# Performance work log

Hardware: AMD Instinct MI355X
Metric: run time of the kernel (lower is better)

Reference implementation:

```python
import jax, jax.numpy as jnp
import numpy as np

B, T, C, NH = 1, 2048, 1024, 16
HS = C // NH            # 64
LEVEL = 6
LMIN = 2 ** LEVEL       # 64 (tail block size)
NB = T // LMIN          # 32 complete sets


def setup_inputs() -> dict:
    key = jax.random.key(0)
    ks = jax.random.split(key, 8)
    def w(k, shape, fan_in):
        return jax.random.normal(k, shape, jnp.float32) / np.sqrt(fan_in)
    return {
        "x": jax.random.normal(ks[0], (B, T, C), jnp.float32),
        "Wq": w(ks[1], (C, C), C),
        "Wk": w(ks[2], (C, C), C),
        "Wv": w(ks[3], (C, C), C),
        "Wkmap": w(ks[4], (HS, HS * HS), HS * HS),
        "bkmap": jnp.zeros((HS,), jnp.float32),
        "Wvmap": w(ks[5], (HS, HS * HS), HS * HS),
        "bvmap": jnp.zeros((HS,), jnp.float32),
        "Wc": w(ks[6], (C, C), C),
        "bc": jnp.zeros((C,), jnp.float32),
    }


def reference(x, Wq, Wk, Wv, Wkmap, bkmap, Wvmap, bvmap, Wc, bc):
    phi = lambda t: jax.nn.elu(t) + 1.0  # feature_map='elu'
    # preprocess: projections + feature map (no q/k normalization)
    q = phi((x @ Wq.T).reshape(B, T, NH, HS))
    k = phi((x @ Wk.T).reshape(B, T, NH, HS))
    v = (x @ Wv.T).reshape(B, T, NH, HS)

    # per-position outer products k_t (x) v_t, grouped into LMIN-sized blocks
    op = jnp.einsum('bthd,bthe->bthde', k, v).reshape(B, NB, LMIN, NH, HS, HS)
    # set feature = final state of linear-attn recurrence over each full block
    set_f = op.sum(axis=2).reshape(B, NB, NH, HS * HS)            # [B,NB,NH,HS^2]
    # tail feature at t = state over [t - t%LMIN, t] = in-block prefix cumsum
    tail_f = jnp.cumsum(op, axis=2).reshape(B, T, NH, HS * HS)    # [B,T,NH,HS^2]

    K = set_f @ Wkmap.T + bkmap      # [B,NB,NH,HS] (k_mapping=True)
    V = set_f @ Wvmap.T + bvmap      # [B,NB,NH,HS] (v_mapping=True)
    K_tail = tail_f @ Wkmap.T + bkmap  # [B,T,NH,HS]
    V_tail = tail_f @ Wvmap.T + bvmap  # [B,T,NH,HS]

    scale = 1.0 / np.sqrt(HS)
    logits = jnp.einsum('bthd,bshd->bhts', q, K) * scale          # [B,NH,T,NB]
    # query t may attend only complete sets strictly before its own block
    mask = jnp.arange(NB)[None, :] < (jnp.arange(T) // LMIN)[:, None]  # [T,NB]
    logits = jnp.where(mask[None, None], logits, -jnp.inf)
    tail_logit = (jnp.einsum('bthd,bthd->bth', q, K_tail) * scale)
    tail_logit = tail_logit.transpose(0, 2, 1)[..., None]         # [B,NH,T,1]

    att = jax.nn.softmax(jnp.concatenate([logits, tail_logit], axis=-1), axis=-1)
    out = (jnp.einsum('bhts,bshd->bhtd', att[..., :-1], V)
           + att[..., -1:] * V_tail.transpose(0, 2, 1, 3))        # [B,NH,T,HS]
    out = out.transpose(0, 2, 1, 3).reshape(B, T, C)
    return out @ Wc.T + bc
```

## Files before the change

### kernel.cpp

```cpp
#include <hip/hip_runtime.h>
#include <hip/hip_bf16.h>
#include <math.h>

typedef __hip_bfloat16 bf16;
typedef __attribute__((ext_vector_type(8))) short short8;
typedef __attribute__((ext_vector_type(4))) float f32x4;

#define C_DIM 1024
#define NHEAD 16
#define HS 64

__device__ __forceinline__ float bf2f(bf16 x) { return __bfloat162float(x); }
__device__ __forceinline__ short bfbits(float x) {
    bf16 h = __float2bfloat16(x);
    return *reinterpret_cast<short*>(&h);
}

__device__ __forceinline__ void gl16(const void* g, void* l) {
    __builtin_amdgcn_global_load_lds(
        (const __attribute__((address_space(1))) unsigned int*)g,
        (__attribute__((address_space(3))) unsigned int*)l, 16, 0, 0);
}

__device__ __forceinline__ void split8(const float* p, short8& h, short8& l) {
    float4 f0 = reinterpret_cast<const float4*>(p)[0];
    float4 f1 = reinterpret_cast<const float4*>(p)[1];
    float vals[8] = {f0.x, f0.y, f0.z, f0.w, f1.x, f1.y, f1.z, f1.w};
#pragma unroll
    for (int j = 0; j < 8; ++j) {
        bf16 hb = __float2bfloat16(vals[j]);
        float r = vals[j] - __bfloat162float(hb);
        h[j] = *reinterpret_cast<short*>(&hb);
        bf16 lb = __float2bfloat16(r);
        l[j] = *reinterpret_cast<short*>(&lb);
    }
}

__device__ __forceinline__ short8* tchunk(bf16* tile, int row, int ch) {
    return reinterpret_cast<short8*>(tile + row * 64 + (((ch) ^ (row & 7)) << 3));
}

__global__ __launch_bounds__(256) void presplit_all_kernel(
    const float* __restrict__ x, const float* __restrict__ Wq,
    const float* __restrict__ Wk, const float* __restrict__ Wv,
    bf16* __restrict__ xh, bf16* __restrict__ xl,
    bf16* __restrict__ wqh, bf16* __restrict__ wql,
    bf16* __restrict__ wkh, bf16* __restrict__ wkl,
    bf16* __restrict__ wvh, bf16* __restrict__ wvl)
{
    int blk = blockIdx.x;
    const float* src; bf16 *dh, *dl; long off;
    if (blk < 1024)      { src = x;  dh = xh;  dl = xl;  off = (long)blk * 2048; }
    else if (blk < 1536) { src = Wq; dh = wqh; dl = wql; off = (long)(blk - 1024) * 2048; }
    else if (blk < 2048) { src = Wk; dh = wkh; dl = wkl; off = (long)(blk - 1536) * 2048; }
    else                 { src = Wv; dh = wvh; dl = wvl; off = (long)(blk - 2048) * 2048; }
    long p = off + threadIdx.x * 8;
    int j = (int)(((p >> 3) ^ (p >> 10)) & 7);
    long dp = (p & ~56l) | ((long)j << 3);
    short8 h8, l8;
    split8(&src[p], h8, l8);
    *reinterpret_cast<short8*>(&dh[dp]) = h8;
    *reinterpret_cast<short8*>(&dl[dp]) = l8;
}

__global__ __launch_bounds__(256) void presplit_wc_kernel(
    const float* __restrict__ Wc, bf16* __restrict__ wch, bf16* __restrict__ wcl)
{
    long p = (long)blockIdx.x * 2048 + threadIdx.x * 8;
    int j = (int)(((p >> 3) ^ (p >> 10)) & 7);
    long dp = (p & ~56l) | ((long)j << 3);
    short8 h8, l8;
    split8(&Wc[p], h8, l8);
    *reinterpret_cast<short8*>(&wch[dp]) = h8;
    *reinterpret_cast<short8*>(&wcl[dp]) = l8;
}

__global__ __launch_bounds__(256) void presplit_wmap_kernel(
    const float* __restrict__ WK, const float* __restrict__ WV, bf16* __restrict__ Wm4)
{
    int d = blockIdx.x;
    int row = threadIdx.x >> 2, e0 = (threadIdx.x & 3) * 16;
    int sw0 = (((e0 >> 3) + 0) ^ (row & 7)) & 7;
    int sw1 = (((e0 >> 3) + 1) ^ (row & 7)) & 7;
    const float* pk = &WK[(long)row * 4096 + d * 64 + e0];
    const float* pv = &WV[(long)row * 4096 + d * 64 + e0];
    long bKh = ((long)(d * 4 + 0) * 64 + row) * 64;
    long bKl = ((long)(d * 4 + 1) * 64 + row) * 64;
    long bVh = ((long)(d * 4 + 2) * 64 + row) * 64;
    long bVl = ((long)(d * 4 + 3) * 64 + row) * 64;
    short8 h8, l8;
    split8(pk, h8, l8);     *(short8*)&Wm4[bKh + sw0*8] = h8; *(short8*)&Wm4[bKl + sw0*8] = l8;
    split8(pk + 8, h8, l8); *(short8*)&Wm4[bKh + sw1*8] = h8; *(short8*)&Wm4[bKl + sw1*8] = l8;
    split8(pv, h8, l8);     *(short8*)&Wm4[bVh + sw0*8] = h8; *(short8*)&Wm4[bVl + sw0*8] = l8;
    split8(pv + 8, h8, l8); *(short8*)&Wm4[bVh + sw1*8] = h8; *(short8*)&Wm4[bVl + sw1*8] = l8;
}

__global__ __launch_bounds__(256) void qkv_kernel(
    const bf16* __restrict__ xh, const bf16* __restrict__ xl,
    const bf16* __restrict__ wqh, const bf16* __restrict__ wql,
    const bf16* __restrict__ wkh, const bf16* __restrict__ wkl,
    const bf16* __restrict__ wvh, const bf16* __restrict__ wvl,
    float* __restrict__ qkv, float* __restrict__ kTg)
{
    __shared__ bf16 lds[32768];
    const int tid = threadIdx.x;
    const int lane = tid & 63, wid = tid >> 6;
    const int wr = wid >> 1, wc = wid & 1;
    const int proj = blockIdx.x >> 3;
    const int n0 = (blockIdx.x & 7) * 128;
    const int m0 = blockIdx.y * 128;
    const bf16* Bhp = proj == 0 ? wqh : (proj == 1 ? wkh : wvh);
    const bf16* Blp = proj == 0 ? wql : (proj == 1 ? wkl : wvl);
    float* C = qkv + (long)proj * 2097152;
    char* lb = reinterpret_cast<char*>(lds);

    f32x4 acc[4][4] = {};
    for (int kt = 0; kt < 16; ++kt) {
        const int k0 = kt << 6;
#pragma unroll
        for (int i = 0; i < 4; ++i) {
            int cc = tid + i * 256;
            int row = cc >> 3, j = cc & 7;
            long soA = (long)(m0 + row) * 1024 + k0 + j * 8;
            long soB = (long)(n0 + row) * 1024 + k0 + j * 8;
            gl16(&xh[soA],  lb + cc * 16);
            gl16(&xl[soA],  lb + 16384 + cc * 16);
            gl16(&Bhp[soB], lb + 32768 + cc * 16);
            gl16(&Blp[soB], lb + 49152 + cc * 16);
        }
        __syncthreads();
#pragma unroll
        for (int kk = 0; kk < 2; ++kk) {
            short8 afh[4], afl[4], bfh[4], bfl[4];
#pragma unroll
            for (int t = 0; t < 4; ++t) {
                int ra = wr * 64 + t * 16 + (lane & 15);
                int rb = wc * 64 + t * 16 + (lane & 15);
                int ch = kk * 4 + (lane >> 4);
                afh[t] = *tchunk(lds, ra, ch);
                afl[t] = *tchunk(lds + 8192, ra, ch);
                bfh[t] = *tchunk(lds + 16384, rb, ch);
                bfl[t] = *tchunk(lds + 24576, rb, ch);
            }
#pragma unroll
            for (int tm = 0; tm < 4; ++tm)
#pragma unroll
                for (int tn = 0; tn < 4; ++tn) {
                    acc[tm][tn] = __builtin_amdgcn_mfma_f32_16x16x32_bf16(
                        afh[tm], bfh[tn], acc[tm][tn], 0, 0, 0);
                    acc[tm][tn] = __builtin_amdgcn_mfma_f32_16x16x32_bf16(
                        afh[tm], bfl[tn], acc[tm][tn], 0, 0, 0);
                    acc[tm][tn] = __builtin_amdgcn_mfma_f32_16x16x32_bf16(
                        afl[tm], bfh[tn], acc[tm][tn], 0, 0, 0);
                }
        }
        __syncthreads();
    }
    if (proj == 1) {
        float* lf = reinterpret_cast<float*>(lds) + wid * 4096;
#pragma unroll
        for (int tm = 0; tm < 4; ++tm)
#pragma unroll
            for (int tn = 0; tn < 4; ++tn)
#pragma unroll
                for (int r = 0; r < 4; ++r) {
                    int s = tm * 16 + (lane >> 4) * 4 + r;
                    int dd = tn * 16 + (lane & 15);
                    float v = acc[tm][tn][r];
                    v = v > 0.f ? v + 1.f : __expf(v);
                    lf[dd * 64 + (s ^ dd)] = v;
                }
        asm volatile("s_waitcnt lgkmcnt(0)" ::: "memory");
        __builtin_amdgcn_sched_barrier(0);
        int pair = (blockIdx.y * 2 + wr) * 16 + ((blockIdx.x & 7) * 2 + wc);
        long pb = (long)pair * 4096;
        int s0 = (lane & 15) * 4;
#pragma unroll
        for (int ii = 0; ii < 16; ++ii) {
            int dd = (lane >> 4) * 16 + ii;
            float4 o;
            o.x = lf[dd * 64 + ((s0 + 0) ^ dd)];
            o.y = lf[dd * 64 + ((s0 + 1) ^ dd)];
            o.z = lf[dd * 64 + ((s0 + 2) ^ dd)];
            o.w = lf[dd * 64 + ((s0 + 3) ^ dd)];
            *reinterpret_cast<float4*>(&kTg[pb + (long)dd * 64 + s0]) = o;
        }
    } else {
#pragma unroll
        for (int tm = 0; tm < 4; ++tm)
#pragma unroll
            for (int tn = 0; tn < 4; ++tn)
#pragma unroll
                for (int r = 0; r < 4; ++r) {
                    int row = m0 + wr * 64 + tm * 16 + (lane >> 4) * 4 + r;
                    int col = n0 + wc * 64 + tn * 16 + (lane & 15);
                    float v = acc[tm][tn][r];
                    if (proj == 0) v = v > 0.f ? v + 1.f : __expf(v);
                    C[(long)row * 1024 + col] = v;
                }
    }
}

__global__ __launch_bounds__(512, 4) void setfeat_kernel(
    const float* __restrict__ kTg, const float* __restrict__ vbuf,
    const bf16* __restrict__ Wm4,
    const float* __restrict__ bkmap, const float* __restrict__ bvmap,
    float* __restrict__ Ktail, float* __restrict__ Vtail,
    float* __restrict__ KsetT, float* __restrict__ Vset)
{
    __shared__ char smem[65536];
    bf16* W0 = reinterpret_cast<bf16*>(smem);
    bf16* W1 = reinterpret_cast<bf16*>(smem + 32768);
    const int tid = threadIdx.x;
    const int grp = tid >> 8, tl = tid & 255;
    const int lane = tl & 63, wid = tl >> 6;
    const int wr = wid >> 1, wc = wid & 1;
    const int pairIdx = blockIdx.x * 2 + grp;
    const int b = pairIdx >> 4, h = pairIdx & 15;
    const long base_kv = ((long)b * 64) * C_DIM + h * HS;
    const float* kp = kTg + (long)pairIdx * 4096;

    float vv0[2][8], vv1[2][8];
#pragma unroll
    for (int kk = 0; kk < 2; ++kk) {
        const float* p0 = &vbuf[base_kv +
            (long)(wr * 32 + (lane & 15)) * C_DIM + kk * 32 + (lane >> 4) * 8];
        const float* p1 = &vbuf[base_kv +
            (long)(wr * 32 + 16 + (lane & 15)) * C_DIM + kk * 32 + (lane >> 4) * 8];
        *reinterpret_cast<float4*>(&vv0[kk][0]) = reinterpret_cast<const float4*>(p0)[0];
        *reinterpret_cast<float4*>(&vv0[kk][4]) = reinterpret_cast<const float4*>(p0)[1];
        *reinterpret_cast<float4*>(&vv1[kk][0]) = reinterpret_cast<const float4*>(p1)[0];
        *reinterpret_cast<float4*>(&vv1[kk][4]) = reinterpret_cast<const float4*>(p1)[1];
    }
    float ks0 = kp[wr * 32 + (lane & 15)];
    float ks1 = kp[wr * 32 + 16 + (lane & 15)];
#pragma unroll
    for (int i = 0; i < 4; ++i) {
        int cc = tid + i * 512;
        gl16(&Wm4[(long)cc * 8], smem + (long)cc * 16);
    }
    f32x4 accK[2][2] = {}, accV[2][2] = {};

    for (int d = 0; d < 64; ++d) {
        bf16* Wcur = (d & 1) ? W1 : W0;
        char* Wnxt = (d & 1) ? smem : smem + 32768;
        __builtin_amdgcn_s_barrier();
        float kn0 = 0.f, kn1 = 0.f;
        if (d < 63) {
            kn0 = kp[(d + 1) * 64 + wr * 32 + (lane & 15)];
            kn1 = kp[(d + 1) * 64 + wr * 32 + 16 + (lane & 15)];
#pragma unroll
            for (int i = 0; i < 4; ++i) {
                int cc = tid + i * 512;
                gl16(&Wm4[(long)(d + 1) * 16384 + (long)cc * 8], Wnxt + (long)cc * 16);
            }
            asm volatile("s_waitcnt vmcnt(6)" ::: "memory");
        } else {
            asm volatile("s_waitcnt vmcnt(0)" ::: "memory");
        }
#pragma unroll
        for (int kk = 0; kk < 2; ++kk) {
            short8 bkh[2], bkl[2], bvh[2], bvl[2];
#pragma unroll
            for (int t = 0; t < 2; ++t) {
                int rb = wc * 32 + t * 16 + (lane & 15);
                int ch = kk * 4 + (lane >> 4);
                bkh[t] = *tchunk(Wcur,         rb, ch);
                bkl[t] = *tchunk(Wcur + 4096,  rb, ch);
                bvh[t] = *tchunk(Wcur + 8192,  rb, ch);
                bvl[t] = *tchunk(Wcur + 12288, rb, ch);
            }
            short8 a0, a1;
#pragma unroll
            for (int j = 0; j < 8; ++j) {
                a0[j] = bfbits(ks0 * vv0[kk][j]);
                a1[j] = bfbits(ks1 * vv1[kk][j]);
            }
#pragma unroll
            for (int tn = 0; tn < 2; ++tn) {
                accK[0][tn] = __builtin_amdgcn_mfma_f32_16x16x32_bf16(a0, bkh[tn], accK[0][tn], 0, 0, 0);
                accK[0][tn] = __builtin_amdgcn_mfma_f32_16x16x32_bf16(a0, bkl[tn], accK[0][tn], 0, 0, 0);
                accK[1][tn] = __builtin_amdgcn_mfma_f32_16x16x32_bf16(a1, bkh[tn], accK[1][tn], 0, 0, 0);
                accK[1][tn] = __builtin_amdgcn_mfma_f32_16x16x32_bf16(a1, bkl[tn], accK[1][tn], 0, 0, 0);
                accV[0][tn] = __builtin_amdgcn_mfma_f32_16x16x32_bf16(a0, bvh[tn], accV[0][tn], 0, 0, 0);
                accV[0][tn] = __builtin_amdgcn_mfma_f32_16x16x32_bf16(a0, bvl[tn], accV[0][tn], 0, 0, 0);
                accV[1][tn] = __builtin_amdgcn_mfma_f32_16x16x32_bf16(a1, bvh[tn], accV[1][tn], 0, 0, 0);
                accV[1][tn] = __builtin_amdgcn_mfma_f32_16x16x32_bf16(a1, bvl[tn], accV[1][tn], 0, 0, 0);
            }
        }
        ks0 = kn0; ks1 = kn1;
    }
    __syncthreads();
    float(*WallK)[64] = reinterpret_cast<float(*)[64]>(smem + grp * 32768);
    float(*WallV)[64] = reinterpret_cast<float(*)[64]>(smem + grp * 32768 + 16384);
#pragma unroll
    for (int tm = 0; tm < 2; ++tm)
#pragma unroll
        for (int tn = 0; tn < 2; ++tn)
#pragma unroll
            for (int r = 0; r < 4; ++r) {
                int row = wr * 32 + tm * 16 + (lane >> 4) * 4 + r;
                int col = wc * 32 + tn * 16 + (lane & 15);
                WallK[row][col] = (tm == 0 ? accK[0][tn][r] : accK[1][tn][r]);
                WallV[row][col] = (tm == 0 ? accV[0][tn][r] : accV[1][tn][r]);
            }
    __syncthreads();
    if (tl < 128) {
        int i = tl & 63;
        bool isV = tl >= 64;
        const float bi = isV ? bvmap[i] : bkmap[i];
        float run = 0.f;
        for (int s = 0; s < 64; ++s) {
            run += isV ? WallV[s][i] : WallK[s][i];
            float val = run + bi;
            long t = (long)b * 64 + s;
            if (isV) Vtail[t * C_DIM + h * HS + i] = val;
            else     Ktail[t * C_DIM + h * HS + i] = val;
            if (s == 63) {
                if (isV) Vset[(b * NHEAD + h) * HS + i] = val;
                else     KsetT[h * 2048 + i * 32 + b] = val;
            }
        }
    }
}

__global__ __launch_bounds__(256) void attn_kernel(
    const float* __restrict__ qbuf, const float* __restrict__ KsetT,
    const float* __restrict__ Vset, const float* __restrict__ Ktail,
    const float* __restrict__ Vtail, bf16* __restrict__ atth, bf16* __restrict__ attl)
{
    __shared__ float qsh[4][64];
    __shared__ float attsh[4][64];
    const int tid = threadIdx.x, lane = tid & 63, wid = tid >> 6;
    const int g = blockIdx.x * 4 + wid;
    const int t = g >> 4, h = g & 15;
    const int nb = t >> 6;
    const float scale = 0.125f;
    const long qoff = (long)t * C_DIM + h * HS;
    float qv = qbuf[qoff + lane];
    qsh[wid][lane] = qv;
    float tp = qv * Ktail[qoff + lane];
    for (int off = 32; off; off >>= 1) tp += __shfl_xor(tp, off, 64);
    __syncthreads();
    float logit = -INFINITY;
    if (lane < nb) {
        float s = 0.f;
        const float* Kp = &KsetT[h * 2048 + lane];
        for (int d = 0; d < 64; ++d) s += qsh[wid][d] * Kp[d * 32];
        logit = s * scale;
    } else if (lane == nb) {
        logit = tp * scale;
    }
    float m = logit;
    for (int off = 32; off; off >>= 1) m = fmaxf(m, __shfl_xor(m, off, 64));
    float e = (lane <= nb) ? __expf(logit - m) : 0.f;
    float sum = e;
    for (int off = 32; off; off >>= 1) sum += __shfl_xor(sum, off, 64);
    attsh[wid][lane] = e / sum;
    __syncthreads();
    float out = 0.f;
    for (int s = 0; s < nb; ++s)
        out += attsh[wid][s] * Vset[(s * NHEAD + h) * HS + lane];
    out += attsh[wid][nb] * Vtail[qoff + lane];
    bf16 hb = __float2bfloat16(out);
    int csw = (((lane >> 3) ^ (t & 7)) << 3) | (lane & 7);
    long po = (long)t * 1024 + h * 64 + csw;
    atth[po] = hb;
    attl[po] = __float2bfloat16(out - bf2f(hb));
}

__global__ __launch_bounds__(256) void gemm_final_kernel(
    const bf16* __restrict__ ah, const bf16* __restrict__ al,
    const bf16* __restrict__ bh, const bf16* __restrict__ bl,
    const float* __restrict__ bias, float* __restrict__ C)
{
    __shared__ bf16 lds[24576];
    const int tid = threadIdx.x;
    const int lane = tid & 63, wid = tid >> 6;
    const int wr = wid >> 1, wc = wid & 1;
    const int m0 = blockIdx.y * 128, n0 = blockIdx.x * 64;
    char* lb = reinterpret_cast<char*>(lds);

    f32x4 acc[4][2] = {};
    for (int kt = 0; kt < 16; ++kt) {
        const int k0 = kt << 6;
#pragma unroll
        for (int i = 0; i < 4; ++i) {
            int cc = tid + i * 256;
            int row = cc >> 3, j = cc & 7;
            long so = (long)(m0 + row) * 1024 + k0 + j * 8;
            gl16(&ah[so], lb + cc * 16);
            gl16(&al[so], lb + 16384 + cc * 16);
        }
#pragma unroll
        for (int i = 0; i < 2; ++i) {
            int cc = tid + i * 256;
            int row = cc >> 3, j = cc & 7;
            long so = (long)(n0 + row) * 1024 + k0 + j * 8;
            gl16(&bh[so], lb + 32768 + cc * 16);
            gl16(&bl[so], lb + 40960 + cc * 16);
        }
        __syncthreads();
#pragma unroll
        for (int kk = 0; kk < 2; ++kk) {
            short8 afh[4], afl[4], bfh[2], bfl[2];
#pragma unroll
            for (int t = 0; t < 4; ++t) {
                int ra = wr * 64 + t * 16 + (lane & 15);
                int ch = kk * 4 + (lane >> 4);
                afh[t] = *tchunk(lds, ra, ch);
                afl[t] = *tchunk(lds + 8192, ra, ch);
            }
#pragma unroll
            for (int t = 0; t < 2; ++t) {
                int rb = wc * 32 + t * 16 + (lane & 15);
                int ch = kk * 4 + (lane >> 4);
                bfh[t] = *tchunk(lds + 16384, rb, ch);
                bfl[t] = *tchunk(lds + 20480, rb, ch);
            }
#pragma unroll
            for (int tm = 0; tm < 4; ++tm)
#pragma unroll
                for (int tn = 0; tn < 2; ++tn) {
                    acc[tm][tn] = __builtin_amdgcn_mfma_f32_16x16x32_bf16(
                        afh[tm], bfh[tn], acc[tm][tn], 0, 0, 0);
                    acc[tm][tn] = __builtin_amdgcn_mfma_f32_16x16x32_bf16(
                        afh[tm], bfl[tn], acc[tm][tn], 0, 0, 0);
                    acc[tm][tn] = __builtin_amdgcn_mfma_f32_16x16x32_bf16(
                        afl[tm], bfh[tn], acc[tm][tn], 0, 0, 0);
                }
        }
        __syncthreads();
    }
#pragma unroll
    for (int tm = 0; tm < 4; ++tm)
#pragma unroll
        for (int tn = 0; tn < 2; ++tn)
#pragma unroll
            for (int r = 0; r < 4; ++r) {
                int row = m0 + wr * 64 + tm * 16 + (lane >> 4) * 4 + r;
                int col = n0 + wc * 32 + tn * 16 + (lane & 15);
                C[(long)row * 1024 + col] = acc[tm][tn][r] + bias[col];
            }
}

extern "C" void kernel_launch(void* const* d_in, const int* in_sizes, int n_in,
                              void* d_out, int out_size, void* d_ws, size_t ws_size,
                              hipStream_t stream)
{
    const float* x     = (const float*)d_in[0];
    const float* Wq    = (const float*)d_in[1];
    const float* Wk    = (const float*)d_in[2];
    const float* Wv    = (const float*)d_in[3];
    const float* Wkmap = (const float*)d_in[4];
    const float* bkmap = (const float*)d_in[5];
    const float* Wvmap = (const float*)d_in[6];
    const float* bvmap = (const float*)d_in[7];
    const float* Wc    = (const float*)d_in[8];
    const float* bc    = (const float*)d_in[9];
    float* out = (float*)d_out;

    char* ws = (char*)d_ws;
    const long MB = 1l << 20;
    float* q   = (float*)(ws + 0 * MB);
    float* kTg = (float*)(ws + 8 * MB);
    float* v   = (float*)(ws + 16 * MB);
    bf16* xh   = (bf16*)(ws + 24 * MB);
    bf16* xl   = (bf16*)(ws + 28 * MB);
    bf16* wqh  = (bf16*)(ws + 32 * MB);
    bf16* wql  = (bf16*)(ws + 34 * MB);
    bf16* wkh  = (bf16*)(ws + 36 * MB);
    bf16* wkl  = (bf16*)(ws + 38 * MB);
    bf16* wvh  = (bf16*)(ws + 40 * MB);
    bf16* wvl  = (bf16*)(ws + 42 * MB);
    bf16* Wm4  = (bf16*)(ws + 44 * MB);
    float* Ktail = (float*)(ws + 24 * MB);
    float* Vtail = (float*)(ws + 32 * MB);
    float* KsetT = (float*)(ws + 40 * MB);
    float* Vset  = (float*)(ws + 41 * MB);
    bf16* atth   = (bf16*)(ws + 8 * MB);
    bf16* attl   = (bf16*)(ws + 12 * MB);
    bf16* wch    = (bf16*)(ws + 44 * MB);
    bf16* wcl    = (bf16*)(ws + 46 * MB);

    presplit_all_kernel<<<2560, 256, 0, stream>>>(x, Wq, Wk, Wv, xh, xl,
                                                  wqh, wql, wkh, wkl, wvh, wvl);
    presplit_wmap_kernel<<<64, 256, 0, stream>>>(Wkmap, Wvmap, Wm4);
    qkv_kernel<<<dim3(24, 16), 256, 0, stream>>>(xh, xl, wqh, wql, wkh, wkl,
                                                 wvh, wvl, q, kTg);
    setfeat_kernel<<<256, 512, 0, stream>>>(kTg, v, Wm4, bkmap, bvmap,
                                            Ktail, Vtail, KsetT, Vset);
    presplit_wc_kernel<<<512, 256, 0, stream>>>(Wc, wch, wcl);
    attn_kernel<<<8192, 256, 0, stream>>>(q, KsetT, Vset, Ktail, Vtail, atth, attl);
    gemm_final_kernel<<<dim3(16, 16), 256, 0, stream>>>(atth, attl, wch, wcl, bc, out);
}
```

Before: 258.7 us.

## Factor k out of set-feature GEMM and split K/V mapping across blocks

```diff
diff --git a/kernel.cpp b/kernel.cpp
--- a/kernel.cpp
+++ b/kernel.cpp
@@ -208,91 +208,98 @@
     float* __restrict__ Ktail, float* __restrict__ Vtail,
     float* __restrict__ KsetT, float* __restrict__ Vset)
 {
-    __shared__ char smem[65536];
+    __shared__ char smem[32768];
     bf16* W0 = reinterpret_cast<bf16*>(smem);
-    bf16* W1 = reinterpret_cast<bf16*>(smem + 32768);
+    bf16* W1 = reinterpret_cast<bf16*>(smem + 16384);
     const int tid = threadIdx.x;
+    const int side = blockIdx.x & 1;
     const int grp = tid >> 8, tl = tid & 255;
     const int lane = tl & 63, wid = tl >> 6;
     const int wr = wid >> 1, wc = wid & 1;
-    const int pairIdx = blockIdx.x * 2 + grp;
+    const int pairIdx = (blockIdx.x >> 1) * 2 + grp;
     const int b = pairIdx >> 4, h = pairIdx & 15;
     const long base_kv = ((long)b * 64) * C_DIM + h * HS;
     const float* kp = kTg + (long)pairIdx * 4096;
-
-    float vv0[2][8], vv1[2][8];
-#pragma unroll
-    for (int kk = 0; kk < 2; ++kk) {
-        const float* p0 = &vbuf[base_kv +
-            (long)(wr * 32 + (lane & 15)) * C_DIM + kk * 32 + (lane >> 4) * 8];
-        const float* p1 = &vbuf[base_kv +
-            (long)(wr * 32 + 16 + (lane & 15)) * C_DIM + kk * 32 + (lane >> 4) * 8];
-        *reinterpret_cast<float4*>(&vv0[kk][0]) = reinterpret_cast<const float4*>(p0)[0];
-        *reinterpret_cast<float4*>(&vv0[kk][4]) = reinterpret_cast<const float4*>(p0)[1];
-        *reinterpret_cast<float4*>(&vv1[kk][0]) = reinterpret_cast<const float4*>(p1)[0];
-        *reinterpret_cast<float4*>(&vv1[kk][4]) = reinterpret_cast<const float4*>(p1)[1];
-    }
-    float ks0 = kp[wr * 32 + (lane & 15)];
-    float ks1 = kp[wr * 32 + 16 + (lane & 15)];
-#pragma unroll
-    for (int i = 0; i < 4; ++i) {
+    const long wsideoff = (long)side * 8192;
+
+    short8 vh[2][2];
+#pragma unroll
+    for (int tm = 0; tm < 2; ++tm)
+#pragma unroll
+        for (int kk = 0; kk < 2; ++kk) {
+            const float* vp = &vbuf[base_kv +
+                (long)(wr * 32 + tm * 16 + (lane & 15)) * C_DIM + kk * 32 + (lane >> 4) * 8];
+            float4 f0 = reinterpret_cast<const float4*>(vp)[0];
+            float4 f1 = reinterpret_cast<const float4*>(vp)[1];
+            float vals[8] = {f0.x, f0.y, f0.z, f0.w, f1.x, f1.y, f1.z, f1.w};
+#pragma unroll
+            for (int j = 0; j < 8; ++j) vh[tm][kk][j] = bfbits(vals[j]);
+        }
+    f32x4 kvc[2];
+#pragma unroll
+    for (int tm = 0; tm < 2; ++tm)
+        kvc[tm] = *reinterpret_cast<const f32x4*>(
+            &kp[wr * 32 + tm * 16 + (lane >> 4) * 4]);
+#pragma unroll
+    for (int i = 0; i < 2; ++i) {
         int cc = tid + i * 512;
-        gl16(&Wm4[(long)cc * 8], smem + (long)cc * 16);
-    }
-    f32x4 accK[2][2] = {}, accV[2][2] = {};
+        gl16(&Wm4[wsideoff + (long)cc * 8], smem + (long)cc * 16);
+    }
+    f32x4 acc[2][2] = {};
+    __syncthreads();
 
     for (int d = 0; d < 64; ++d) {
         bf16* Wcur = (d & 1) ? W1 : W0;
-        char* Wnxt = (d & 1) ? smem : smem + 32768;
+        char* Wnxt = (d & 1) ? smem : smem + 16384;
         __builtin_amdgcn_s_barrier();
-        float kn0 = 0.f, kn1 = 0.f;
+        f32x4 kvn[2] = {};
         if (d < 63) {
-            kn0 = kp[(d + 1) * 64 + wr * 32 + (lane & 15)];
-            kn1 = kp[(d + 1) * 64 + wr * 32 + 16 + (lane & 15)];
-#pragma unroll
-            for (int i = 0; i < 4; ++i) {
+#pragma unroll
+            for (int i = 0; i < 2; ++i) {
                 int cc = tid + i * 512;
-                gl16(&Wm4[(long)(d + 1) * 16384 + (long)cc * 8], Wnxt + (long)cc * 16);
-            }
-            asm volatile("s_waitcnt vmcnt(6)" ::: "memory");
+                gl16(&Wm4[(long)(d + 1) * 16384 + wsideoff + (long)cc * 8],
+                     Wnxt + (long)cc * 16);
+            }
+#pragma unroll
+            for (int tm = 0; tm < 2; ++tm)
+                kvn[tm] = *reinterpret_cast<const f32x4*>(
+                    &kp[(d + 1) * 64 + wr * 32 + tm * 16 + (lane >> 4) * 4]);
+            asm volatile("s_waitcnt vmcnt(4)" ::: "memory");
         } else {
             asm volatile("s_waitcnt vmcnt(0)" ::: "memory");
         }
+        f32x4 G[2][2] = {};
 #pragma unroll
         for (int kk = 0; kk < 2; ++kk) {
-            short8 bkh[2], bkl[2], bvh[2], bvl[2];
+            short8 bh_[2], bl_[2];
 #pragma unroll
             for (int t = 0; t < 2; ++t) {
                 int rb = wc * 32 + t * 16 + (lane & 15);
                 int ch = kk * 4 + (lane >> 4);
-                bkh[t] = *tchunk(Wcur,         rb, ch);
-                bkl[t] = *tchunk(Wcur + 4096,  rb, ch);
-                bvh[t] = *tchunk(Wcur + 8192,  rb, ch);
-                bvl[t] = *tchunk(Wcur + 12288, rb, ch);
-            }
-            short8 a0, a1;
-#pragma unroll
-            for (int j = 0; j < 8; ++j) {
-                a0[j] = bfbits(ks0 * vv0[kk][j]);
-                a1[j] = bfbits(ks1 * vv1[kk][j]);
-            }
-#pragma unroll
-            for (int tn = 0; tn < 2; ++tn) {
-                accK[0][tn] = __builtin_amdgcn_mfma_f32_16x16x32_bf16(a0, bkh[tn], accK[0][tn], 0, 0, 0);
-                accK[0][tn] = __builtin_amdgcn_mfma_f32_16x16x32_bf16(a0, bkl[tn], accK[0][tn], 0, 0, 0);
-                accK[1][tn] = __builtin_amdgcn_mfma_f32_16x16x32_bf16(a1, bkh[tn], accK[1][tn], 0, 0, 0);
-                accK[1][tn] = __builtin_amdgcn_mfma_f32_16x16x32_bf16(a1, bkl[tn], accK[1][tn], 0, 0, 0);
-                accV[0][tn] = __builtin_amdgcn_mfma_f32_16x16x32_bf16(a0, bvh[tn], accV[0][tn], 0, 0, 0);
-                accV[0][tn] = __builtin_amdgcn_mfma_f32_16x16x32_bf16(a0, bvl[tn], accV[0][tn], 0, 0, 0);
-                accV[1][tn] = __builtin_amdgcn_mfma_f32_16x16x32_bf16(a1, bvh[tn], accV[1][tn], 0, 0, 0);
-                accV[1][tn] = __builtin_amdgcn_mfma_f32_16x16x32_bf16(a1, bvl[tn], accV[1][tn], 0, 0, 0);
-            }
-        }
-        ks0 = kn0; ks1 = kn1;
+                bh_[t] = *tchunk(Wcur,        rb, ch);
+                bl_[t] = *tchunk(Wcur + 4096, rb, ch);
+            }
+#pragma unroll
+            for (int tm = 0; tm < 2; ++tm)
+#pragma unroll
+                for (int tn = 0; tn < 2; ++tn) {
+                    G[tm][tn] = __builtin_amdgcn_mfma_f32_16x16x32_bf16(
+                        vh[tm][kk], bh_[tn], G[tm][tn], 0, 0, 0);
+                    G[tm][tn] = __builtin_amdgcn_mfma_f32_16x16x32_bf16(
+                        vh[tm][kk], bl_[tn], G[tm][tn], 0, 0, 0);
+                }
+        }
+#pragma unroll
+        for (int tm = 0; tm < 2; ++tm)
+#pragma unroll
+            for (int tn = 0; tn < 2; ++tn)
+#pragma unroll
+                for (int r = 0; r < 4; ++r)
+                    acc[tm][tn][r] += kvc[tm][r] * G[tm][tn][r];
+        kvc[0] = kvn[0]; kvc[1] = kvn[1];
     }
     __syncthreads();
-    float(*WallK)[64] = reinterpret_cast<float(*)[64]>(smem + grp * 32768);
-    float(*WallV)[64] = reinterpret_cast<float(*)[64]>(smem + grp * 32768 + 16384);
+    float(*Wall)[64] = reinterpret_cast<float(*)[64]>(smem + grp * 16384);
 #pragma unroll
     for (int tm = 0; tm < 2; ++tm)
 #pragma unroll
@@ -301,24 +308,22 @@
             for (int r = 0; r < 4; ++r) {
                 int row = wr * 32 + tm * 16 + (lane >> 4) * 4 + r;
                 int col = wc * 32 + tn * 16 + (lane & 15);
-                WallK[row][col] = (tm == 0 ? accK[0][tn][r] : accK[1][tn][r]);
-                WallV[row][col] = (tm == 0 ? accV[0][tn][r] : accV[1][tn][r]);
+                Wall[row][col] = acc[tm][tn][r];
             }
     __syncthreads();
-    if (tl < 128) {
-        int i = tl & 63;
-        bool isV = tl >= 64;
-        const float bi = isV ? bvmap[i] : bkmap[i];
+    if (tl < 64) {
+        int i = tl;
+        const float bi = side ? bvmap[i] : bkmap[i];
         float run = 0.f;
         for (int s = 0; s < 64; ++s) {
-            run += isV ? WallV[s][i] : WallK[s][i];
+            run += Wall[s][i];
             float val = run + bi;
             long t = (long)b * 64 + s;
-            if (isV) Vtail[t * C_DIM + h * HS + i] = val;
-            else     Ktail[t * C_DIM + h * HS + i] = val;
+            if (side) Vtail[t * C_DIM + h * HS + i] = val;
+            else      Ktail[t * C_DIM + h * HS + i] = val;
             if (s == 63) {
-                if (isV) Vset[(b * NHEAD + h) * HS + i] = val;
-                else     KsetT[h * 2048 + i * 32 + b] = val;
+                if (side) Vset[(b * NHEAD + h) * HS + i] = val;
+                else      KsetT[h * 2048 + i * 32 + b] = val;
             }
         }
     }
@@ -488,7 +493,7 @@
     presplit_wmap_kernel<<<64, 256, 0, stream>>>(Wkmap, Wvmap, Wm4);
     qkv_kernel<<<dim3(24, 16), 256, 0, stream>>>(xh, xl, wqh, wql, wkh, wkl,
                                                  wvh, wvl, q, kTg);
-    setfeat_kernel<<<256, 512, 0, stream>>>(kTg, v, Wm4, bkmap, bvmap,
+    setfeat_kernel<<<512, 512, 0, stream>>>(kTg, v, Wm4, bkmap, bvmap,
                                             Ktail, Vtail, KsetT, Vset);
     presplit_wc_kernel<<<512, 256, 0, stream>>>(Wc, wch, wcl);
     attn_kernel<<<8192, 256, 0, stream>>>(q, KsetT, Vset, Ktail, Vtail, atth, attl);
```

Result: faster. 253.3 us (-2.1%).
